# Optimization experiments

Measured on AMD Instinct MI355X. Metric: run time of the kernel, lower is better.

Reference implementation:

```python
import jax, jax.numpy as jnp
import numpy as np

DIM = 256

def setup_inputs() -> dict:
    key = jax.random.key(0)
    ks = jax.random.split(key, 7)
    B, S, D = 8, 4096, DIM
    scale = 1.0 / np.sqrt(D)
    x = jax.random.normal(ks[0], (B, S, D), dtype=jnp.float32)
    # torch Linear: y = x @ W.T + b, W is [out, in]
    Wq = jax.random.normal(ks[1], (D, D), dtype=jnp.float32) * scale
    Wk = jax.random.normal(ks[2], (D, D), dtype=jnp.float32) * scale
    Wv = jax.random.normal(ks[3], (D, D), dtype=jnp.float32) * scale
    bq = jax.random.normal(ks[4], (D,), dtype=jnp.float32) * 0.01
    bk = jax.random.normal(ks[5], (D,), dtype=jnp.float32) * 0.01
    bv = jax.random.normal(ks[6], (D,), dtype=jnp.float32) * 0.01
    return {"x": x, "Wq": Wq, "bq": bq, "Wk": Wk, "bk": bk, "Wv": Wv, "bv": bv}

def reference(x, Wq, bq, Wk, bk, Wv, bv):
    D = x.shape[-1]
    scale = D ** -0.5
    q = jnp.einsum('bsd,ed->bse', x, Wq) + bq  # [B,S,D]
    k = jnp.einsum('bsd,ed->bse', x, Wk) + bk
    v = jnp.einsum('bsd,ed->bse', x, Wv) + bv
    attn = jnp.einsum('bqd,bkd->bqk', q, k) * scale  # [B,S,S]
    attn = jax.nn.softmax(attn, axis=-1)
    return x + jnp.einsum('bqk,bkd->bqd', attn, v)
```

## Files before the change

### kernel.cpp

```cpp
#include <hip/hip_runtime.h>
#include <hip/hip_bf16.h>

typedef __attribute__((ext_vector_type(8))) short bf16x8;
typedef __attribute__((ext_vector_type(4))) float f32x4;

#define MFMA16(a, b, c) __builtin_amdgcn_mfma_f32_16x16x32_bf16(a, b, c, 0, 0, 0)

__device__ __forceinline__ short f2bf(float f) {
    union { __hip_bfloat16 h; short s; } u;
    u.h = __float2bfloat16(f);
    return u.s;
}

__device__ __forceinline__ bf16x8 cvt8(const float* __restrict__ p) {
    f32x4 a = *reinterpret_cast<const f32x4*>(p);
    f32x4 b = *reinterpret_cast<const f32x4*>(p + 4);
    bf16x8 r;
    r[0] = f2bf(a[0]); r[1] = f2bf(a[1]); r[2] = f2bf(a[2]); r[3] = f2bf(a[3]);
    r[4] = f2bf(b[0]); r[5] = f2bf(b[1]); r[6] = f2bf(b[2]); r[7] = f2bf(b[3]);
    return r;
}

typedef __attribute__((address_space(1))) const unsigned int g_u32;
typedef __attribute__((address_space(3))) unsigned int l_u32;
__device__ __forceinline__ void gld16(const void* g, void* l) {
    __builtin_amdgcn_global_load_lds((g_u32*)(g), (l_u32*)(l), 16, 0, 0);
}

__global__ void wcvt_kernel(const float* __restrict__ Wq, const float* __restrict__ Wk,
                            const float* __restrict__ Wv, short* __restrict__ Wb)
{
    int t = blockIdx.x * 256 + threadIdx.x;
    int idx = t * 8;
    const float* src = idx < 65536 ? Wq + idx
                     : (idx < 131072 ? Wk + (idx - 65536) : Wv + (idx - 131072));
    *reinterpret_cast<bf16x8*>(Wb + idx) = cvt8(src);
}

__global__ __launch_bounds__(256, 2) void qkv_kernel(
    const float* __restrict__ x, const short* __restrict__ Wb,
    const float* __restrict__ bq, const float* __restrict__ bk, const float* __restrict__ bv,
    short* __restrict__ qo, short* __restrict__ ko, short* __restrict__ vto)
{
    const int wave = threadIdx.x >> 6;
    const int lane = threadIdx.x & 63;
    const int l15 = lane & 15, l4 = lane >> 4;
    const int row0  = blockIdx.x * 64;
    const int wrow0 = row0 + wave * 16;

    bf16x8 af[8];
    const float* __restrict__ xr = x + (size_t)(wrow0 + l15) * 256 + l4 * 8;
#pragma unroll
    for (int kc = 0; kc < 8; ++kc) af[kc] = cvt8(xr + kc * 32);

    __shared__ short tile[64][264];

    for (int proj = 0; proj < 3; ++proj) {
        const short* __restrict__ W = Wb + proj * 65536;
        const float* __restrict__ bias = proj == 0 ? bq : (proj == 1 ? bk : bv);

        f32x4 acc[16];
#pragma unroll
        for (int nf = 0; nf < 16; ++nf) { f32x4 z = {0.f,0.f,0.f,0.f}; acc[nf] = z; }

#pragma unroll
        for (int nf = 0; nf < 16; ++nf) {
            const short* __restrict__ wr = W + (nf * 16 + l15) * 256 + l4 * 8;
#pragma unroll
            for (int kc = 0; kc < 8; ++kc) {
                bf16x8 bfrag = *reinterpret_cast<const bf16x8*>(wr + kc * 32);
                acc[nf] = MFMA16(af[kc], bfrag, acc[nf]);
            }
        }

        if (proj) __syncthreads();
#pragma unroll
        for (int nf = 0; nf < 16; ++nf) {
            int col = nf * 16 + l15;
            float bv_ = bias[col];
#pragma unroll
            for (int r = 0; r < 4; ++r)
                tile[wave * 16 + l4 * 4 + r][col] = f2bf(acc[nf][r] + bv_);
        }
        __syncthreads();

        if (proj < 2) {
            short* __restrict__ dst = (proj == 0 ? qo : ko) + (size_t)row0 * 256;
#pragma unroll
            for (int i = 0; i < 8; ++i) {
                int chunk = threadIdx.x + i * 256;
                int r = chunk >> 5, cc = chunk & 31;
                bf16x8 v = *reinterpret_cast<const bf16x8*>(&tile[r][cc * 8]);
                *reinterpret_cast<bf16x8*>(dst + chunk * 8) = v;
            }
        } else {
            int d  = threadIdx.x;
            int bb = row0 >> 12;
            int s0 = row0 & 4095;
            short* __restrict__ dst = vto + ((size_t)bb * 256 + d) * 4096 + s0;
#pragma unroll
            for (int i = 0; i < 8; ++i) {
                bf16x8 v;
#pragma unroll
                for (int j = 0; j < 8; ++j) v[j] = tile[i * 8 + j][d];
                *reinterpret_cast<bf16x8*>(dst + i * 8) = v;
            }
        }
    }
}

__global__ __launch_bounds__(512, 2) void attn_kernel(
    const short* __restrict__ q, const short* __restrict__ k,
    const short* __restrict__ vt, const float* __restrict__ x,
    float* __restrict__ out)
{
    const int id = blockIdx.x;
    const int b = id & 7, qt = id >> 3;
    const int tid = threadIdx.x;
    const int wave = tid >> 6, lane = tid & 63;
    const int l15 = lane & 15, l4 = lane >> 4;
    const int qrow0 = qt * 128 + wave * 16;

    const short* __restrict__ qb = q  + (size_t)b * 4096 * 256;
    const short* __restrict__ kb = k  + (size_t)b * 4096 * 256;
    const short* __restrict__ vb = vt + (size_t)b * 256 * 4096;

    __shared__ short klds[2][16384];
    __shared__ short vlds[16384];
    __shared__ short plds[8][16][72];

    bf16x8 qf[8];
    const short* __restrict__ qr = qb + (size_t)(qrow0 + l15) * 256 + l4 * 8;
#pragma unroll
    for (int kc = 0; kc < 8; ++kc)
        qf[kc] = *reinterpret_cast<const bf16x8*>(qr + kc * 32);

    f32x4 o[16];
#pragma unroll
    for (int df = 0; df < 16; ++df) { f32x4 z = {0.f,0.f,0.f,0.f}; o[df] = z; }
    float m2[4]   = {-INFINITY, -INFINITY, -INFINITY, -INFINITY};
    float lsum[4] = {0.f, 0.f, 0.f, 0.f};

    const float cs = 0.0625f * 1.44269504f;

    bf16x8 vreg[4];

#define STAGE_K(KV, BUF)                                                      \
    {                                                                         \
        _Pragma("unroll")                                                     \
        for (int i = 0; i < 4; ++i) {                                         \
            int c = i * 512 + tid;                                            \
            int nf = c >> 9, kc = (c >> 6) & 7, rr = (c >> 2) & 15, c4 = c & 3;\
            gld16(kb + (size_t)((KV) + nf * 16 + rr) * 256 + (kc * 4 + c4) * 8,\
                  &klds[BUF][c * 8]);                                         \
        }                                                                     \
    }
#define LOAD_V(KV)                                                            \
    {                                                                         \
        _Pragma("unroll")                                                     \
        for (int i = 0; i < 4; ++i) {                                         \
            int c = i * 512 + tid;                                            \
            int df = c >> 7, k2 = (c >> 6) & 1, rr = (c >> 2) & 15, c4 = c & 3;\
            vreg[i] = *reinterpret_cast<const bf16x8*>(                       \
                vb + (size_t)(df * 16 + rr) * 4096 + (KV) + (k2 * 4 + c4) * 8);\
        }                                                                     \
    }
#define WRITE_V()                                                             \
    {                                                                         \
        _Pragma("unroll")                                                     \
        for (int i = 0; i < 4; ++i) {                                         \
            int c = i * 512 + tid;                                            \
            *reinterpret_cast<bf16x8*>(&vlds[c * 8]) = vreg[i];               \
        }                                                                     \
    }

    STAGE_K(0, 0);
    LOAD_V(0);
    __syncthreads();
    WRITE_V();
    __syncthreads();

    short (*pw)[72] = plds[wave];

    for (int t = 0; t < 64; ++t) {
        const int kv = t * 64;
        const int cur = t & 1;
        if (t < 63) { STAGE_K(kv + 64, cur ^ 1); LOAD_V(kv + 64); }

        f32x4 s[4];
#pragma unroll
        for (int nf = 0; nf < 4; ++nf) { f32x4 z = {0.f,0.f,0.f,0.f}; s[nf] = z; }
        const short* __restrict__ kbase = klds[cur];
#pragma unroll
        for (int nf = 0; nf < 4; ++nf)
#pragma unroll
            for (int kc = 0; kc < 8; ++kc) {
                bf16x8 kf = *reinterpret_cast<const bf16x8*>(
                    kbase + (nf * 512 + kc * 64 + l15 * 4 + l4) * 8);
                s[nf] = MFMA16(qf[kc], kf, s[nf]);
            }

        float tt[4][4];
#pragma unroll
        for (int nf = 0; nf < 4; ++nf)
#pragma unroll
            for (int r = 0; r < 4; ++r) tt[nf][r] = s[nf][r] * cs;

        float mx[4];
#pragma unroll
        for (int r = 0; r < 4; ++r) {
            float v = fmaxf(fmaxf(tt[0][r], tt[1][r]), fmaxf(tt[2][r], tt[3][r]));
#pragma unroll
            for (int d = 1; d < 16; d <<= 1) v = fmaxf(v, __shfl_xor(v, d));
            mx[r] = v;
        }
        bool grow = (mx[0] > m2[0]) | (mx[1] > m2[1]) | (mx[2] > m2[2]) | (mx[3] > m2[3]);
        if (__any(grow)) {
#pragma unroll
            for (int r = 0; r < 4; ++r) {
                float mn = fmaxf(m2[r], mx[r]);
                float al = exp2f(m2[r] - mn);
                m2[r] = mn;
                lsum[r] *= al;
#pragma unroll
                for (int df = 0; df < 16; ++df) o[df][r] *= al;
            }
        }

        float p[4][4];
#pragma unroll
        for (int r = 0; r < 4; ++r) {
            float rs = 0.f;
#pragma unroll
            for (int nf = 0; nf < 4; ++nf) {
                float pv_ = exp2f(tt[nf][r] - m2[r]);
                p[nf][r] = pv_;
                rs += pv_;
            }
#pragma unroll
            for (int d = 1; d < 16; d <<= 1) rs += __shfl_xor(rs, d);
            lsum[r] += rs;
        }

#pragma unroll
        for (int nf = 0; nf < 4; ++nf)
#pragma unroll
            for (int r = 0; r < 4; ++r)
                pw[l4 * 4 + r][nf * 16 + l15] = f2bf(p[nf][r]);

        bf16x8 pf[2];
#pragma unroll
        for (int kc2 = 0; kc2 < 2; ++kc2)
            pf[kc2] = *reinterpret_cast<const bf16x8*>(&pw[l15][kc2 * 32 + l4 * 8]);

#pragma unroll
        for (int df = 0; df < 16; ++df)
#pragma unroll
            for (int kc2 = 0; kc2 < 2; ++kc2) {
                bf16x8 vf = *reinterpret_cast<const bf16x8*>(
                    vlds + (df * 128 + kc2 * 64 + l15 * 4 + l4) * 8);
                o[df] = MFMA16(pf[kc2], vf, o[df]);
            }

        __syncthreads();
        if (t < 63) WRITE_V();
        __syncthreads();
    }

#pragma unroll
    for (int r = 0; r < 4; ++r) {
        float inv = 1.0f / lsum[r];
        size_t row = (size_t)b * 4096 + qrow0 + l4 * 4 + r;
#pragma unroll
        for (int df = 0; df < 16; ++df) {
            int col = df * 16 + l15;
            out[row * 256 + col] = o[df][r] * inv + x[row * 256 + col];
        }
    }
#undef STAGE_K
#undef LOAD_V
#undef WRITE_V
}

extern "C" void kernel_launch(void* const* d_in, const int* in_sizes, int n_in,
                              void* d_out, int out_size, void* d_ws, size_t ws_size,
                              hipStream_t stream) {
    const float* x  = (const float*)d_in[0];
    const float* Wq = (const float*)d_in[1];
    const float* bq = (const float*)d_in[2];
    const float* Wk = (const float*)d_in[3];
    const float* bk = (const float*)d_in[4];
    const float* Wv = (const float*)d_in[5];
    const float* bv = (const float*)d_in[6];
    float* out = (float*)d_out;

    char* ws = (char*)d_ws;
    short* qb  = (short*)ws;
    short* kb  = (short*)(ws + (size_t)16 * 1024 * 1024);
    short* vtb = (short*)(ws + (size_t)32 * 1024 * 1024);
    short* Wb = (short*)d_out;

    wcvt_kernel<<<96, 256, 0, stream>>>(Wq, Wk, Wv, Wb);

    qkv_kernel<<<512, 256, 0, stream>>>(x, Wb, bq, bk, bv, qb, kb, vtb);

    attn_kernel<<<256, 512, 0, stream>>>(qb, kb, vtb, x, out);
}
```

Measured before the change: 353.4 us.

## Switch to 32x32x16 MFMA tiles in QKV and attention kernels

Rewrites the QKV projection and attention kernels to use 32x32x16 bf16 MFMA with 32 rows per wave instead of 16x16x32 with 16 rows. Attention drops to 4 waves per block and double-buffers V in LDS via direct global-to-LDS loads instead of staging through registers, which removes the second barrier per iteration. The row sum is now reduced across lanes only once, after the loop. Q and K projection outputs go straight to global memory and skip the LDS tile. The aim is fewer MFMA issues and more data reuse per wave, at the cost of more registers, lower occupancy and scattered 2-byte global stores for Q and K.

```diff
diff --git a/kernel.cpp b/kernel.cpp
--- a/kernel.cpp
+++ b/kernel.cpp
@@ -3,8 +3,9 @@
 
 typedef __attribute__((ext_vector_type(8))) short bf16x8;
 typedef __attribute__((ext_vector_type(4))) float f32x4;
-
-#define MFMA16(a, b, c) __builtin_amdgcn_mfma_f32_16x16x32_bf16(a, b, c, 0, 0, 0)
+typedef __attribute__((ext_vector_type(16))) float f32x16;
+
+#define MFMA32(a, b, c) __builtin_amdgcn_mfma_f32_32x32x16_bf16(a, b, c, 0, 0, 0)
 
 __device__ __forceinline__ short f2bf(float f) {
     union { __hip_bfloat16 h; short s; } u;
@@ -42,64 +43,66 @@
     const float* __restrict__ bq, const float* __restrict__ bk, const float* __restrict__ bv,
     short* __restrict__ qo, short* __restrict__ ko, short* __restrict__ vto)
 {
-    const int wave = threadIdx.x >> 6;
-    const int lane = threadIdx.x & 63;
-    const int l15 = lane & 15, l4 = lane >> 4;
-    const int row0  = blockIdx.x * 64;
-    const int wrow0 = row0 + wave * 16;
-
-    bf16x8 af[8];
-    const float* __restrict__ xr = x + (size_t)(wrow0 + l15) * 256 + l4 * 8;
-#pragma unroll
-    for (int kc = 0; kc < 8; ++kc) af[kc] = cvt8(xr + kc * 32);
-
-    __shared__ short tile[64][264];
+    const int wave = threadIdx.x >> 6, lane = threadIdx.x & 63;
+    const int l31 = lane & 31, h = lane >> 5;
+    const int row0 = blockIdx.x * 128;
+    const int wrow = row0 + wave * 32;
+
+    bf16x8 af[16];
+    const float* __restrict__ xr = x + (size_t)(wrow + l31) * 256 + h * 8;
+#pragma unroll
+    for (int kc = 0; kc < 16; ++kc) af[kc] = cvt8(xr + kc * 16);
+
+    __shared__ short tile[128][264];
 
     for (int proj = 0; proj < 3; ++proj) {
         const short* __restrict__ W = Wb + proj * 65536;
         const float* __restrict__ bias = proj == 0 ? bq : (proj == 1 ? bk : bv);
 
-        f32x4 acc[16];
-#pragma unroll
-        for (int nf = 0; nf < 16; ++nf) { f32x4 z = {0.f,0.f,0.f,0.f}; acc[nf] = z; }
-
-#pragma unroll
-        for (int nf = 0; nf < 16; ++nf) {
-            const short* __restrict__ wr = W + (nf * 16 + l15) * 256 + l4 * 8;
-#pragma unroll
-            for (int kc = 0; kc < 8; ++kc) {
-                bf16x8 bfrag = *reinterpret_cast<const bf16x8*>(wr + kc * 32);
-                acc[nf] = MFMA16(af[kc], bfrag, acc[nf]);
-            }
-        }
-
-        if (proj) __syncthreads();
-#pragma unroll
-        for (int nf = 0; nf < 16; ++nf) {
-            int col = nf * 16 + l15;
-            float bv_ = bias[col];
-#pragma unroll
-            for (int r = 0; r < 4; ++r)
-                tile[wave * 16 + l4 * 4 + r][col] = f2bf(acc[nf][r] + bv_);
-        }
-        __syncthreads();
+        f32x16 acc[8];
+#pragma unroll
+        for (int df = 0; df < 8; ++df)
+#pragma unroll
+            for (int e = 0; e < 16; ++e) acc[df][e] = 0.f;
+
+#pragma unroll
+        for (int kc = 0; kc < 16; ++kc)
+#pragma unroll
+            for (int df = 0; df < 8; ++df) {
+                bf16x8 bfr = *reinterpret_cast<const bf16x8*>(
+                    W + (df * 32 + l31) * 256 + kc * 16 + h * 8);
+                acc[df] = MFMA32(af[kc], bfr, acc[df]);
+            }
 
         if (proj < 2) {
-            short* __restrict__ dst = (proj == 0 ? qo : ko) + (size_t)row0 * 256;
-#pragma unroll
-            for (int i = 0; i < 8; ++i) {
-                int chunk = threadIdx.x + i * 256;
-                int r = chunk >> 5, cc = chunk & 31;
-                bf16x8 v = *reinterpret_cast<const bf16x8*>(&tile[r][cc * 8]);
-                *reinterpret_cast<bf16x8*>(dst + chunk * 8) = v;
+            short* __restrict__ dst = proj == 0 ? qo : ko;
+#pragma unroll
+            for (int df = 0; df < 8; ++df) {
+                int col = df * 32 + l31;
+                float bv_ = bias[col];
+#pragma unroll
+                for (int rg = 0; rg < 16; ++rg) {
+                    int r = (rg & 3) + 8 * (rg >> 2) + 4 * h;
+                    dst[(size_t)(wrow + r) * 256 + col] = f2bf(acc[df][rg] + bv_);
+                }
             }
         } else {
-            int d  = threadIdx.x;
-            int bb = row0 >> 12;
-            int s0 = row0 & 4095;
+#pragma unroll
+            for (int df = 0; df < 8; ++df) {
+                int col = df * 32 + l31;
+                float bv_ = bias[col];
+#pragma unroll
+                for (int rg = 0; rg < 16; ++rg) {
+                    int r = (rg & 3) + 8 * (rg >> 2) + 4 * h;
+                    tile[wave * 32 + r][col] = f2bf(acc[df][rg] + bv_);
+                }
+            }
+            __syncthreads();
+            int d = threadIdx.x;
+            int bb = row0 >> 12, s0 = row0 & 4095;
             short* __restrict__ dst = vto + ((size_t)bb * 256 + d) * 4096 + s0;
 #pragma unroll
-            for (int i = 0; i < 8; ++i) {
+            for (int i = 0; i < 16; ++i) {
                 bf16x8 v;
 #pragma unroll
                 for (int j = 0; j < 8; ++j) v[j] = tile[i * 8 + j][d];
@@ -109,7 +112,7 @@
     }
 }
 
-__global__ __launch_bounds__(512, 2) void attn_kernel(
+__global__ __launch_bounds__(256, 1) void attn_kernel(
     const short* __restrict__ q, const short* __restrict__ k,
     const short* __restrict__ vt, const float* __restrict__ x,
     float* __restrict__ out)
@@ -118,168 +121,155 @@
     const int b = id & 7, qt = id >> 3;
     const int tid = threadIdx.x;
     const int wave = tid >> 6, lane = tid & 63;
-    const int l15 = lane & 15, l4 = lane >> 4;
-    const int qrow0 = qt * 128 + wave * 16;
+    const int l31 = lane & 31, h = lane >> 5;
+    const int qrow0 = qt * 128 + wave * 32;
 
     const short* __restrict__ qb = q  + (size_t)b * 4096 * 256;
     const short* __restrict__ kb = k  + (size_t)b * 4096 * 256;
     const short* __restrict__ vb = vt + (size_t)b * 256 * 4096;
 
     __shared__ short klds[2][16384];
-    __shared__ short vlds[16384];
-    __shared__ short plds[8][16][72];
-
-    bf16x8 qf[8];
-    const short* __restrict__ qr = qb + (size_t)(qrow0 + l15) * 256 + l4 * 8;
-#pragma unroll
-    for (int kc = 0; kc < 8; ++kc)
-        qf[kc] = *reinterpret_cast<const bf16x8*>(qr + kc * 32);
-
-    f32x4 o[16];
-#pragma unroll
-    for (int df = 0; df < 16; ++df) { f32x4 z = {0.f,0.f,0.f,0.f}; o[df] = z; }
-    float m2[4]   = {-INFINITY, -INFINITY, -INFINITY, -INFINITY};
-    float lsum[4] = {0.f, 0.f, 0.f, 0.f};
+    __shared__ short vlds[2][16384];
+    __shared__ short plds[4][32][72];
+
+    bf16x8 qf[16];
+    const short* __restrict__ qr = qb + (size_t)(qrow0 + l31) * 256 + h * 8;
+#pragma unroll
+    for (int kc = 0; kc < 16; ++kc)
+        qf[kc] = *reinterpret_cast<const bf16x8*>(qr + kc * 16);
+
+    f32x16 o[8];
+#pragma unroll
+    for (int df = 0; df < 8; ++df)
+#pragma unroll
+        for (int e = 0; e < 16; ++e) o[df][e] = 0.f;
+
+    float m2[16], ls[16];
+#pragma unroll
+    for (int rg = 0; rg < 16; ++rg) { m2[rg] = -INFINITY; ls[rg] = 0.f; }
 
     const float cs = 0.0625f * 1.44269504f;
 
-    bf16x8 vreg[4];
-
-#define STAGE_K(KV, BUF)                                                      \
-    {                                                                         \
-        _Pragma("unroll")                                                     \
-        for (int i = 0; i < 4; ++i) {                                         \
-            int c = i * 512 + tid;                                            \
-            int nf = c >> 9, kc = (c >> 6) & 7, rr = (c >> 2) & 15, c4 = c & 3;\
-            gld16(kb + (size_t)((KV) + nf * 16 + rr) * 256 + (kc * 4 + c4) * 8,\
-                  &klds[BUF][c * 8]);                                         \
-        }                                                                     \
-    }
-#define LOAD_V(KV)                                                            \
-    {                                                                         \
-        _Pragma("unroll")                                                     \
-        for (int i = 0; i < 4; ++i) {                                         \
-            int c = i * 512 + tid;                                            \
-            int df = c >> 7, k2 = (c >> 6) & 1, rr = (c >> 2) & 15, c4 = c & 3;\
-            vreg[i] = *reinterpret_cast<const bf16x8*>(                       \
-                vb + (size_t)(df * 16 + rr) * 4096 + (KV) + (k2 * 4 + c4) * 8);\
-        }                                                                     \
-    }
-#define WRITE_V()                                                             \
-    {                                                                         \
-        _Pragma("unroll")                                                     \
-        for (int i = 0; i < 4; ++i) {                                         \
-            int c = i * 512 + tid;                                            \
-            *reinterpret_cast<bf16x8*>(&vlds[c * 8]) = vreg[i];               \
-        }                                                                     \
-    }
+#define STAGE_K(KV, BUF)                                                       \
+    { _Pragma("unroll")                                                        \
+      for (int i = 0; i < 8; ++i) {                                            \
+          int c = i * 256 + tid;                                               \
+          int nf = c >> 10, kc = (c >> 6) & 15, l = c & 63;                    \
+          gld16(kb + (size_t)((KV) + nf * 32 + (l & 31)) * 256                 \
+                    + kc * 16 + (l >> 5) * 8,                                  \
+                &klds[BUF][c * 8]);                                            \
+      } }
+#define STAGE_V(KV, BUF)                                                       \
+    { _Pragma("unroll")                                                        \
+      for (int i = 0; i < 8; ++i) {                                            \
+          int c = i * 256 + tid;                                               \
+          int df = c >> 8, k2 = (c >> 6) & 3, l = c & 63;                      \
+          gld16(vb + (size_t)(df * 32 + (l & 31)) * 4096 + (KV)                \
+                    + k2 * 16 + (l >> 5) * 8,                                  \
+                &vlds[BUF][c * 8]);                                            \
+      } }
 
     STAGE_K(0, 0);
-    LOAD_V(0);
+    STAGE_V(0, 0);
     __syncthreads();
-    WRITE_V();
-    __syncthreads();
 
     short (*pw)[72] = plds[wave];
 
     for (int t = 0; t < 64; ++t) {
-        const int kv = t * 64;
-        const int cur = t & 1;
-        if (t < 63) { STAGE_K(kv + 64, cur ^ 1); LOAD_V(kv + 64); }
-
-        f32x4 s[4];
-#pragma unroll
-        for (int nf = 0; nf < 4; ++nf) { f32x4 z = {0.f,0.f,0.f,0.f}; s[nf] = z; }
+        const int kv = t * 64, cur = t & 1;
+        if (t < 63) { STAGE_K(kv + 64, cur ^ 1); STAGE_V(kv + 64, cur ^ 1); }
+
+        f32x16 s0v, s1v;
+#pragma unroll
+        for (int e = 0; e < 16; ++e) { s0v[e] = 0.f; s1v[e] = 0.f; }
         const short* __restrict__ kbase = klds[cur];
 #pragma unroll
-        for (int nf = 0; nf < 4; ++nf)
-#pragma unroll
-            for (int kc = 0; kc < 8; ++kc) {
-                bf16x8 kf = *reinterpret_cast<const bf16x8*>(
-                    kbase + (nf * 512 + kc * 64 + l15 * 4 + l4) * 8);
-                s[nf] = MFMA16(qf[kc], kf, s[nf]);
-            }
-
-        float tt[4][4];
-#pragma unroll
-        for (int nf = 0; nf < 4; ++nf)
-#pragma unroll
-            for (int r = 0; r < 4; ++r) tt[nf][r] = s[nf][r] * cs;
-
-        float mx[4];
-#pragma unroll
-        for (int r = 0; r < 4; ++r) {
-            float v = fmaxf(fmaxf(tt[0][r], tt[1][r]), fmaxf(tt[2][r], tt[3][r]));
-#pragma unroll
-            for (int d = 1; d < 16; d <<= 1) v = fmaxf(v, __shfl_xor(v, d));
-            mx[r] = v;
-        }
-        bool grow = (mx[0] > m2[0]) | (mx[1] > m2[1]) | (mx[2] > m2[2]) | (mx[3] > m2[3]);
-        if (__any(grow)) {
-#pragma unroll
-            for (int r = 0; r < 4; ++r) {
-                float mn = fmaxf(m2[r], mx[r]);
-                float al = exp2f(m2[r] - mn);
-                m2[r] = mn;
-                lsum[r] *= al;
-#pragma unroll
-                for (int df = 0; df < 16; ++df) o[df][r] *= al;
-            }
-        }
-
-        float p[4][4];
-#pragma unroll
-        for (int r = 0; r < 4; ++r) {
-            float rs = 0.f;
-#pragma unroll
-            for (int nf = 0; nf < 4; ++nf) {
-                float pv_ = exp2f(tt[nf][r] - m2[r]);
-                p[nf][r] = pv_;
-                rs += pv_;
-            }
-#pragma unroll
-            for (int d = 1; d < 16; d <<= 1) rs += __shfl_xor(rs, d);
-            lsum[r] += rs;
-        }
-
-#pragma unroll
-        for (int nf = 0; nf < 4; ++nf)
-#pragma unroll
-            for (int r = 0; r < 4; ++r)
-                pw[l4 * 4 + r][nf * 16 + l15] = f2bf(p[nf][r]);
-
-        bf16x8 pf[2];
-#pragma unroll
-        for (int kc2 = 0; kc2 < 2; ++kc2)
-            pf[kc2] = *reinterpret_cast<const bf16x8*>(&pw[l15][kc2 * 32 + l4 * 8]);
-
-#pragma unroll
-        for (int df = 0; df < 16; ++df)
-#pragma unroll
-            for (int kc2 = 0; kc2 < 2; ++kc2) {
-                bf16x8 vf = *reinterpret_cast<const bf16x8*>(
-                    vlds + (df * 128 + kc2 * 64 + l15 * 4 + l4) * 8);
-                o[df] = MFMA16(pf[kc2], vf, o[df]);
-            }
+        for (int kc = 0; kc < 16; ++kc) {
+            bf16x8 k0 = *reinterpret_cast<const bf16x8*>(kbase + (kc * 64 + lane) * 8);
+            bf16x8 k1 = *reinterpret_cast<const bf16x8*>(kbase + (1024 + kc * 64 + lane) * 8);
+            s0v = MFMA32(qf[kc], k0, s0v);
+            s1v = MFMA32(qf[kc], k1, s1v);
+        }
+
+        float tt0[16], tt1[16], mxa[16];
+#pragma unroll
+        for (int rg = 0; rg < 16; ++rg) { tt0[rg] = s0v[rg] * cs; tt1[rg] = s1v[rg] * cs; }
+#pragma unroll
+        for (int rg = 0; rg < 16; ++rg) {
+            float v = fmaxf(tt0[rg], tt1[rg]);
+#pragma unroll
+            for (int d = 1; d < 32; d <<= 1) v = fmaxf(v, __shfl_xor(v, d));
+            mxa[rg] = v;
+        }
+        bool g = false;
+#pragma unroll
+        for (int rg = 0; rg < 16; ++rg) g = g || (mxa[rg] > m2[rg]);
+        if (__any(g)) {
+            float al[16];
+#pragma unroll
+            for (int rg = 0; rg < 16; ++rg) {
+                float mn = fmaxf(m2[rg], mxa[rg]);
+                float a = exp2f(m2[rg] - mn);
+                m2[rg] = mn;
+                ls[rg] *= a;
+                al[rg] = a;
+            }
+#pragma unroll
+            for (int df = 0; df < 8; ++df)
+#pragma unroll
+                for (int rg = 0; rg < 16; ++rg) o[df][rg] *= al[rg];
+        }
+
+#pragma unroll
+        for (int rg = 0; rg < 16; ++rg) {
+            float p0 = exp2f(tt0[rg] - m2[rg]);
+            float p1 = exp2f(tt1[rg] - m2[rg]);
+            ls[rg] += p0 + p1;
+            int r = (rg & 3) + 8 * (rg >> 2) + 4 * h;
+            pw[r][l31]      = f2bf(p0);
+            pw[r][32 + l31] = f2bf(p1);
+        }
+        bf16x8 pf0 = *reinterpret_cast<const bf16x8*>(&pw[l31][h * 8]);
+        bf16x8 pf1 = *reinterpret_cast<const bf16x8*>(&pw[l31][16 + h * 8]);
+        bf16x8 pf2 = *reinterpret_cast<const bf16x8*>(&pw[l31][32 + h * 8]);
+        bf16x8 pf3 = *reinterpret_cast<const bf16x8*>(&pw[l31][48 + h * 8]);
+
+        const short* __restrict__ vbase = vlds[cur];
+#pragma unroll
+        for (int df = 0; df < 8; ++df) {
+            bf16x8 v0 = *reinterpret_cast<const bf16x8*>(vbase + (df * 256 + lane) * 8);
+            bf16x8 v1 = *reinterpret_cast<const bf16x8*>(vbase + (df * 256 + 64 + lane) * 8);
+            bf16x8 v2 = *reinterpret_cast<const bf16x8*>(vbase + (df * 256 + 128 + lane) * 8);
+            bf16x8 v3 = *reinterpret_cast<const bf16x8*>(vbase + (df * 256 + 192 + lane) * 8);
+            o[df] = MFMA32(pf0, v0, o[df]);
+            o[df] = MFMA32(pf1, v1, o[df]);
+            o[df] = MFMA32(pf2, v2, o[df]);
+            o[df] = MFMA32(pf3, v3, o[df]);
+        }
 
         __syncthreads();
-        if (t < 63) WRITE_V();
-        __syncthreads();
-    }
-
-#pragma unroll
-    for (int r = 0; r < 4; ++r) {
-        float inv = 1.0f / lsum[r];
-        size_t row = (size_t)b * 4096 + qrow0 + l4 * 4 + r;
-#pragma unroll
-        for (int df = 0; df < 16; ++df) {
-            int col = df * 16 + l15;
-            out[row * 256 + col] = o[df][r] * inv + x[row * 256 + col];
+    }
+
+    float inv[16];
+#pragma unroll
+    for (int rg = 0; rg < 16; ++rg) {
+        float v = ls[rg];
+#pragma unroll
+        for (int d = 1; d < 32; d <<= 1) v += __shfl_xor(v, d);
+        inv[rg] = 1.0f / v;
+    }
+#pragma unroll
+    for (int df = 0; df < 8; ++df) {
+        int col = df * 32 + l31;
+#pragma unroll
+        for (int rg = 0; rg < 16; ++rg) {
+            int r = (rg & 3) + 8 * (rg >> 2) + 4 * h;
+            size_t row = (size_t)b * 4096 + qrow0 + r;
+            out[row * 256 + col] = o[df][rg] * inv[rg] + x[row * 256 + col];
         }
     }
 #undef STAGE_K
-#undef LOAD_V
-#undef WRITE_V
+#undef STAGE_V
 }
 
 extern "C" void kernel_launch(void* const* d_in, const int* in_sizes, int n_in,
@@ -298,11 +288,11 @@
     short* qb  = (short*)ws;
     short* kb  = (short*)(ws + (size_t)16 * 1024 * 1024);
     short* vtb = (short*)(ws + (size_t)32 * 1024 * 1024);
-    short* Wb = (short*)d_out;
+    short* Wb  = (short*)d_out;
 
     wcvt_kernel<<<96, 256, 0, stream>>>(Wq, Wk, Wv, Wb);
 
-    qkv_kernel<<<512, 256, 0, stream>>>(x, Wb, bq, bk, bv, qb, kb, vtb);
-
-    attn_kernel<<<256, 512, 0, stream>>>(qb, kb, vtb, x, out);
-}
+    qkv_kernel<<<256, 256, 0, stream>>>(x, Wb, bq, bk, bv, qb, kb, vtb);
+
+    attn_kernel<<<256, 256, 0, stream>>>(qb, kb, vtb, x, out);
+}
```

Measured after the change: 607.9 us. 72.0% more time.
